# Kernel optimization log

Hardware: AMD Instinct MI355X
Metric: run time of the kernel (lower is better)

Reference implementation:

```python
import jax, jax.numpy as jnp
import numpy as np

S, B, H = 2048, 2, 2048
NH = 16
HD = H // NH  # 128
ROPE_BASE = 10000.0


def _rope_cos_sin(seq_len, dim, dtype):
    inv_freq = 1.0 / (ROPE_BASE ** (jnp.arange(0, dim, 2, dtype=jnp.float32) / dim))
    t = jnp.arange(seq_len, dtype=jnp.float32)
    freqs = jnp.outer(t, inv_freq)            # [S, dim/2]
    emb = jnp.concatenate([freqs, freqs], -1)  # [S, dim]
    return jnp.cos(emb).astype(dtype), jnp.sin(emb).astype(dtype)


def _rotate_half(x):
    x1, x2 = jnp.split(x, 2, axis=-1)
    return jnp.concatenate([-x2, x1], axis=-1)


def setup_inputs() -> dict:
    key = jax.random.key(0)
    k1, k2, k3 = jax.random.split(key, 3)
    hidden_states = jax.random.normal(k1, (S, B, H), dtype=jnp.float32)
    w_qkv = jax.random.normal(k2, (3 * H, H), dtype=jnp.float32) * (1.0 / np.sqrt(H))
    w_out = jax.random.normal(k3, (H, H), dtype=jnp.float32) * (1.0 / np.sqrt(H))
    return {"hidden_states": hidden_states, "w_qkv": w_qkv, "w_out": w_out}


def reference(hidden_states, w_qkv, w_out):
    seq_len, batch, _ = hidden_states.shape
    # QKV projection (nn.Linear: x @ W^T), bias=False
    qkv = jnp.einsum('sbh,oh->sbo', hidden_states, w_qkv)
    qkv = qkv.reshape(seq_len, batch, 3, NH, HD)
    q, k, v = qkv[:, :, 0], qkv[:, :, 1], qkv[:, :, 2]  # [S, B, NH, HD]

    cos, sin = _rope_cos_sin(seq_len, HD, hidden_states.dtype)
    cos = cos[:, None, None, :]
    sin = sin[:, None, None, :]
    q = q * cos + _rotate_half(q) * sin
    k = k * cos + _rotate_half(k) * sin

    # [S, B, NH, HD] -> [B, NH, S, HD]
    q = q.transpose(1, 2, 0, 3)
    k = k.transpose(1, 2, 0, 3)
    v = v.transpose(1, 2, 0, 3)

    scale = 1.0 / np.sqrt(HD)
    scores = jnp.einsum('bhqd,bhkd->bhqk', q, k) * scale
    causal = jnp.tril(jnp.ones((seq_len, seq_len), dtype=bool))
    scores = jnp.where(causal, scores, jnp.finfo(scores.dtype).min)
    probs = jax.nn.softmax(scores, axis=-1)
    attn = jnp.einsum('bhqk,bhkd->bhqd', probs, v)  # [B, NH, S, HD]

    # [B, NH, S, HD] -> [S, B, NH*HD]
    out = attn.transpose(2, 0, 1, 3).reshape(seq_len, batch, -1)
    out = jnp.einsum('sbh,oh->sbo', out, w_out)
    return out
```

## Files before the change

kernel.cpp:

```cpp
#include <hip/hip_runtime.h>
#include <hip/hip_bf16.h>

typedef __attribute__((ext_vector_type(8))) short bf16x8;
typedef __attribute__((ext_vector_type(8))) short s16x8;
typedef __attribute__((ext_vector_type(4))) float f32x4;
typedef __attribute__((ext_vector_type(4))) int i32x4;

#define SEQ 2048
#define BATCH 2
#define HID 2048
#define NH 16
#define HD 128
#define QKVN 6144

static __device__ __forceinline__ short f2bf(float f) {
    union { float f; unsigned u; } v; v.f = f;
    unsigned r = (v.u + 0x7FFFu + ((v.u >> 16) & 1u)) >> 16;
    return (short)r;
}

static __device__ __forceinline__ void gload_lds16(const short* g, short* l) {
    __builtin_amdgcn_global_load_lds((const __attribute__((address_space(1))) void*)g,
                                     (__attribute__((address_space(3))) void*)l, 16, 0, 0);
}

static __device__ __forceinline__ void cvt_body(const float* in, short* out, int i) {
    f32x4 a = *(const f32x4*)(in + (size_t)i * 8);
    f32x4 b = *(const f32x4*)(in + (size_t)i * 8 + 4);
    s16x8 o = { f2bf(a.x), f2bf(a.y), f2bf(a.z), f2bf(a.w),
                f2bf(b.x), f2bf(b.y), f2bf(b.z), f2bf(b.w) };
    *(s16x8*)(out + (size_t)i * 8) = o;
}

__global__ void cvt_kernel(const float* __restrict__ in, short* __restrict__ out, int n8) {
    const int i = blockIdx.x * 256 + threadIdx.x;
    if (i >= n8) return;
    cvt_body(in, out, i);
}

__global__ void cvt2_kernel(const float* __restrict__ inA, short* __restrict__ outA,
                            const float* __restrict__ inB, short* __restrict__ outB) {
    const int bid = blockIdx.x;
    if (bid < 4096) cvt_body(inA, outA, bid * 256 + threadIdx.x);
    else            cvt_body(inB, outB, (bid - 4096) * 256 + threadIdx.x);
}

#define G128_STAGE_A(BUF, HA, KK) do { \
    const short* _s = ((HA) ? aS1 : aS0) + (size_t)(KK) * 64; \
    short* _d = lds + (BUF) * 16384 + (HA) * 8192 + w * 512; \
    gload_lds16(_s, _d); \
    gload_lds16(_s + (size_t)128 * K, _d + 4096); \
} while (0)

#define G128_STAGE_B(BUF, HB, KK) do { \
    const short* _s = ((HB) ? bS1 : bS0) + (size_t)(KK) * 64; \
    short* _d = lds + 32768 + (BUF) * 8192 + (HB) * 4096 + w * 512; \
    gload_lds16(_s, _d); \
} while (0)

#define G128_LOAD_A(HA) do { \
    const short* _p = lds + bufR * 16384 + (HA) * 8192; \
    _Pragma("unroll") \
    for (int mm = 0; mm < 2; ++mm) { \
        aR[mm][0] = *(const bf16x8*)(_p + aOff0 + mm * 1024); \
        aR[mm][1] = *(const bf16x8*)(_p + aOff1 + mm * 1024); \
    } \
} while (0)

#define G128_LOAD_B(HB) do { \
    const short* _p = lds + 32768 + bufR * 8192 + (HB) * 4096; \
    _Pragma("unroll") \
    for (int nn = 0; nn < 2; ++nn) { \
        bR[(HB) * 2 + nn][0] = *(const bf16x8*)(_p + bOff0 + nn * 1024); \
        bR[(HB) * 2 + nn][1] = *(const bf16x8*)(_p + bOff1 + nn * 1024); \
    } \
} while (0)

#define G128_MFMA(HA, HB) do { \
    _Pragma("unroll") \
    for (int mm = 0; mm < 2; ++mm) { \
        _Pragma("unroll") \
        for (int nn = 0; nn < 2; ++nn) { \
            f32x4 _c = acc[(HA) * 2 + mm][(HB) * 2 + nn]; \
            _c = __builtin_amdgcn_mfma_f32_16x16x32_bf16(aR[mm][0], bR[(HB) * 2 + nn][0], _c, 0, 0, 0); \
            _c = __builtin_amdgcn_mfma_f32_16x16x32_bf16(aR[mm][1], bR[(HB) * 2 + nn][1], _c, 0, 0, 0); \
            acc[(HA) * 2 + mm][(HB) * 2 + nn] = _c; \
        } \
    } \
} while (0)

template<bool STORE_BF16>
__global__ __launch_bounds__(512, 2)
void gemm128n(const short* __restrict__ A, const short* __restrict__ B,
              void* __restrict__ Cp, int N, int K) {
    __shared__ short lds[49152];

    const int tid = threadIdx.x;
    const int mBase = blockIdx.y * 256;
    const int nBase = blockIdx.x * 128;
    const int w = tid >> 6, lane = tid & 63, quad = lane >> 4, l15 = lane & 15;
    const int wm = w >> 1, wn = w & 1;

    const int kcol = 8 * ((tid & 7) ^ ((tid >> 3) & 7));
    const int srow = ((tid >> 3) & 15) + (tid >> 7) * 32;
    const short* aS0 = A + (size_t)(mBase + srow) * K + kcol;
    const short* aS1 = aS0 + (size_t)16 * K;
    const short* bS0 = B + (size_t)(nBase + srow) * K + kcol;
    const short* bS1 = bS0 + (size_t)16 * K;

    const int cs0 = (quad * 8) ^ ((l15 & 7) << 3);
    const int aOff0 = (l15 + wm * 32) * 64 + cs0;
    const int aOff1 = aOff0 ^ 32;
    const int bOff0 = (l15 + wn * 32) * 64 + cs0;
    const int bOff1 = bOff0 ^ 32;

    const int NK = K >> 6;
    f32x4 acc[4][4] = {};
    bf16x8 aR[2][2], bR[4][2];

    G128_STAGE_A(0, 0, 0); G128_STAGE_B(0, 0, 0); G128_STAGE_B(0, 1, 0); G128_STAGE_A(0, 1, 0);
    G128_STAGE_A(1, 0, 1); G128_STAGE_B(1, 0, 1); G128_STAGE_B(1, 1, 1);
    asm volatile("s_waitcnt vmcnt(4)" ::: "memory");
    __builtin_amdgcn_s_barrier();

    int bufR = 0;
    for (int k = 0; k < NK; ++k) {
        const int kk1 = (k + 1 < NK) ? k + 1 : NK - 1;
        const int kk2 = (k + 2 < NK) ? k + 2 : NK - 1;
        G128_LOAD_A(0);
        G128_LOAD_B(0);
        G128_STAGE_A(bufR ^ 1, 1, kk1);
        asm volatile("s_waitcnt lgkmcnt(4)" ::: "memory");
        __builtin_amdgcn_s_barrier();
        asm volatile("s_waitcnt lgkmcnt(0)" ::: "memory");
        __builtin_amdgcn_s_setprio(1);
        G128_MFMA(0, 0);
        __builtin_amdgcn_s_setprio(0);
        __builtin_amdgcn_s_barrier();
        G128_LOAD_B(1);
        G128_STAGE_A(bufR, 0, kk2);
        __builtin_amdgcn_s_barrier();
        asm volatile("s_waitcnt lgkmcnt(0)" ::: "memory");
        __builtin_amdgcn_s_setprio(1);
        G128_MFMA(0, 1);
        __builtin_amdgcn_s_setprio(0);
        __builtin_amdgcn_s_barrier();
        G128_LOAD_A(1);
        G128_STAGE_B(bufR, 0, kk2);
        __builtin_amdgcn_s_barrier();
        asm volatile("s_waitcnt lgkmcnt(0)" ::: "memory");
        __builtin_amdgcn_s_setprio(1);
        G128_MFMA(1, 1);
        __builtin_amdgcn_s_setprio(0);
        __builtin_amdgcn_s_barrier();
        G128_STAGE_B(bufR, 1, kk2);
        asm volatile("s_waitcnt vmcnt(4)" ::: "memory");
        __builtin_amdgcn_s_barrier();
        __builtin_amdgcn_s_setprio(1);
        G128_MFMA(1, 0);
        __builtin_amdgcn_s_setprio(0);
        __builtin_amdgcn_s_barrier();
        bufR ^= 1;
    }
    asm volatile("s_waitcnt vmcnt(0)" ::: "memory");

    #pragma unroll
    for (int af = 0; af < 4; ++af) {
        const int ha = af >> 1, mm = af & 1;
        const int row0 = mBase + wm * 64 + (2 * mm + ha) * 16 + quad * 4;
        #pragma unroll
        for (int bg = 0; bg < 4; ++bg) {
            const int hb = bg >> 1, nn = bg & 1;
            const int col = nBase + wn * 64 + (2 * nn + hb) * 16 + l15;
            #pragma unroll
            for (int r = 0; r < 4; ++r) {
                if (STORE_BF16)
                    ((short*)Cp)[(size_t)(row0 + r) * N + col] = f2bf(acc[af][bg][r]);
                else
                    ((float*)Cp)[(size_t)(row0 + r) * N + col] = acc[af][bg][r];
            }
        }
    }
}

__global__ void rope_kernel(short* __restrict__ qkv) {
    const int tid = blockIdx.x * 256 + threadIdx.x;
    const int d     = tid & 63;
    const int h     = (tid >> 6) & 15;
    const int which = (tid >> 10) & 1;
    const int b     = (tid >> 11) & 1;
    const int s     = tid >> 12;

    const size_t base = (size_t)(s * 2 + b) * QKVN + which * 2048 + h * 128;
    const float inv_freq = expf(-((float)(2 * d) * (1.0f / 128.0f)) * 9.210340371976184f);
    float sn, cs;
    sincosf((float)s * inv_freq, &sn, &cs);
    const float post = (which == 0) ? 0.08838834764831845f : 1.0f;

    union { unsigned u; float f; } x1, x2;
    x1.u = ((unsigned)(unsigned short)qkv[base + d]) << 16;
    x2.u = ((unsigned)(unsigned short)qkv[base + d + 64]) << 16;
    qkv[base + d]      = f2bf((x1.f * cs - x2.f * sn) * post);
    qkv[base + d + 64] = f2bf((x2.f * cs + x1.f * sn) * post);
}

__global__ void vtrans_kernel(const short* __restrict__ qkv, short* __restrict__ vT) {
    __shared__ short T[64][72];
    const int s0 = blockIdx.x * 64, d0 = blockIdx.y * 64;
    const int bh = blockIdx.z;
    const int b = bh >> 4, h = bh & 15;
    const int t = threadIdx.x;

    #pragma unroll
    for (int p = 0; p < 2; ++p) {
        const int sl = (t >> 3) + p * 32;
        const int dl = (t & 7) * 8;
        *(i32x4*)&T[sl][dl] =
            *(const i32x4*)(qkv + (size_t)((s0 + sl) * 2 + b) * QKVN + 4096 + h * 128 + d0 + dl);
    }
    __syncthreads();
    #pragma unroll
    for (int p = 0; p < 2; ++p) {
        const int dl = (t >> 3) + p * 32;
        const int sl = (t & 7) * 8;
        short tmp[8];
        #pragma unroll
        for (int j = 0; j < 8; ++j) tmp[j] = T[sl + j][dl];
        *(i32x4*)(vT + ((size_t)bh * 128 + d0 + dl) * 2048 + s0 + sl) = *(i32x4*)tmp;
    }
}

__global__ __launch_bounds__(256, 2)
void attn_kernel(const short* __restrict__ qkv, const short* __restrict__ vT,
                 short* __restrict__ out) {
    __shared__ short lds[40960];

    const int bx = blockIdx.x;
    const int h = blockIdx.y, b = blockIdx.z;
    const int Aq = (bx & 1) ? (bx >> 1) : (15 - (bx >> 1));
    const int qt = b ? (15 - Aq) : Aq;
    const int tid = threadIdx.x;
    const int w = tid >> 6, lane = tid & 63, quad = lane >> 4, l15 = lane & 15;
    const int bh = b * 16 + h;
    const int cswz = (l15 & 7) << 3;

    bf16x8 aq[2][4];
    #pragma unroll
    for (int m = 0; m < 2; ++m) {
        const short* qbase =
            qkv + (size_t)((qt * 128 + w * 32 + m * 16 + l15) * 2 + b) * QKVN + h * 128;
        #pragma unroll
        for (int c = 0; c < 4; ++c)
            aq[m][c] = *(const bf16x8*)(qbase + c * 32 + quad * 8);
    }

    f32x4 oacc[2][8] = {};
    float lpart[2][4] = {};

    const short* kSrc0 = qkv + (size_t)((w * 16 + (lane >> 4)) * 2 + b) * QKVN
                       + 2048 + h * 128 + ((lane & 15) ^ (lane >> 4)) * 8;
    const short* kSrc1 = qkv + (size_t)((w * 16 + 4 + (lane >> 4)) * 2 + b) * QKVN
                       + 2048 + h * 128 + ((lane & 15) ^ (4 | (lane >> 4))) * 8;
    const short* vSrc = vT + ((size_t)bh * 128 + w * 32 + (lane >> 3)) * 2048
                      + ((lane & 7) ^ ((lane >> 3) & 7)) * 8;
    short* kDst = lds + w * 2048;
    short* vDst = lds + 16384 + w * 2048;

#define STAGE_KV(BUF, KK0) do { \
    const size_t kAdv = (size_t)(KK0) * 2 * QKVN; \
    short* _kd = kDst + (BUF) * 8192; \
    short* _vd = vDst + (BUF) * 8192; \
    gload_lds16(kSrc0 + kAdv,                  _kd); \
    gload_lds16(kSrc1 + kAdv,                  _kd + 512); \
    gload_lds16(kSrc0 + kAdv + 16 * QKVN,      _kd + 1024); \
    gload_lds16(kSrc1 + kAdv + 16 * QKVN,      _kd + 1536); \
    gload_lds16(vSrc + (KK0),                  _vd); \
    gload_lds16(vSrc + (KK0) + 8 * 2048,       _vd + 512); \
    gload_lds16(vSrc + (KK0) + 16 * 2048,      _vd + 1024); \
    gload_lds16(vSrc + (KK0) + 24 * 2048,      _vd + 1536); \
} while (0)

    const int nChunks = 2 * qt + 2;

    STAGE_KV(0, 0);
    asm volatile("s_waitcnt vmcnt(0)" ::: "memory");
    __builtin_amdgcn_s_barrier();

    for (int ck = 0; ck < nChunks; ++ck) {
        const int cur = ck & 1;
        const int kk0 = ck * 64;
        if (ck + 1 < nChunks) STAGE_KV(cur ^ 1, kk0 + 64);

        const short* Kc = lds + cur * 8192;
        const short* Vc = lds + 16384 + cur * 8192;
        short* Pw = lds + 32768 + w * 2048;

        f32x4 sc4[2][4] = {};
        #pragma unroll
        for (int c = 0; c < 4; ++c) {
            const int cb = (c * 32 + quad * 8) ^ cswz;
            #pragma unroll
            for (int n = 0; n < 4; ++n) {
                bf16x8 bk = *(const bf16x8*)(Kc + (n * 16 + l15) * 128 + cb);
                sc4[0][n] = __builtin_amdgcn_mfma_f32_16x16x32_bf16(aq[0][c], bk, sc4[0][n], 0, 0, 0);
                sc4[1][n] = __builtin_amdgcn_mfma_f32_16x16x32_bf16(aq[1][c], bk, sc4[1][n], 0, 0, 0);
            }
        }

        const bool diag = (ck >= 2 * qt);
        #pragma unroll
        for (int m = 0; m < 2; ++m) {
            const int rowbase = qt * 128 + w * 32 + m * 16 + quad * 4;
            #pragma unroll
            for (int r = 0; r < 4; ++r) {
                const int prow = m * 16 + quad * 4 + r;
                const int pswz = ((quad * 4 + r) & 7) << 3;
                #pragma unroll
                for (int n = 0; n < 4; ++n) {
                    float sv = sc4[m][n][r];
                    if (diag && (kk0 + n * 16 + l15 > rowbase + r)) sv = -1e30f;
                    const float p = __expf(sv);
                    lpart[m][r] += p;
                    Pw[prow * 64 + ((n * 16 + l15) ^ pswz)] = f2bf(p);
                }
            }
        }

        #pragma unroll
        for (int kp2 = 0; kp2 < 2; ++kp2) {
            const int cb = (kp2 * 32 + quad * 8) ^ cswz;
            bf16x8 ap0 = *(const bf16x8*)(Pw + l15 * 64 + cb);
            bf16x8 ap1 = *(const bf16x8*)(Pw + (16 + l15) * 64 + cb);
            #pragma unroll
            for (int dt = 0; dt < 8; ++dt) {
                bf16x8 bv = *(const bf16x8*)(Vc + (dt * 16 + l15) * 64 + cb);
                oacc[0][dt] = __builtin_amdgcn_mfma_f32_16x16x32_bf16(ap0, bv, oacc[0][dt], 0, 0, 0);
                oacc[1][dt] = __builtin_amdgcn_mfma_f32_16x16x32_bf16(ap1, bv, oacc[1][dt], 0, 0, 0);
            }
        }

        asm volatile("s_waitcnt vmcnt(0)" ::: "memory");
        __builtin_amdgcn_s_barrier();
    }
#undef STAGE_KV

    #pragma unroll
    for (int m = 0; m < 2; ++m) {
        const int rowbase = qt * 128 + w * 32 + m * 16 + quad * 4;
        #pragma unroll
        for (int r = 0; r < 4; ++r) {
            float l = lpart[m][r];
            #pragma unroll
            for (int off = 1; off < 16; off <<= 1)
                l += __shfl_xor(l, off);
            const float inv_l = 1.0f / l;
            const size_t obase = (size_t)((rowbase + r) * 2 + b) * HID + h * 128;
            #pragma unroll
            for (int dt = 0; dt < 8; ++dt)
                out[obase + dt * 16 + l15] = f2bf(oacc[m][dt][r] * inv_l);
        }
    }
}

extern "C" void kernel_launch(void* const* d_in, const int* in_sizes, int n_in,
                              void* d_out, int out_size, void* d_ws, size_t ws_size,
                              hipStream_t stream) {
    const float* hidden = (const float*)d_in[0];
    const float* w_qkv  = (const float*)d_in[1];
    const float* w_out  = (const float*)d_in[2];
    float* out = (float*)d_out;

    short* qkv     = (short*)d_ws;
    short* attnb   = qkv + (size_t)4096 * QKVN;
    short* wqkv_bf = attnb + (size_t)4096 * HID;
    short* wout_bf = wqkv_bf;
    short* hbf     = wqkv_bf + (size_t)QKVN * HID;
    short* vT      = hbf;

    dim3 blk(256);
    cvt2_kernel<<<dim3(4096 + 6144), blk, 0, stream>>>(hidden, hbf, w_qkv, wqkv_bf);
    gemm128n<true><<<dim3(QKVN / 128, 4096 / 256), dim3(512), 0, stream>>>(
        hbf, wqkv_bf, qkv, QKVN, HID);
    cvt_kernel<<<dim3(2048), blk, 0, stream>>>(w_out, wout_bf, 2048 * 256);
    rope_kernel<<<dim3((SEQ * BATCH * 2 * NH * (HD / 2)) / 256), blk, 0, stream>>>(qkv);
    vtrans_kernel<<<dim3(SEQ / 64, HD / 64, BATCH * NH), blk, 0, stream>>>(qkv, vT);
    attn_kernel<<<dim3(SEQ / 128, NH, BATCH), blk, 0, stream>>>(qkv, vT, attnb);
    gemm128n<false><<<dim3(HID / 128, 4096 / 256), dim3(512), 0, stream>>>(
        attnb, wout_bf, out, HID, HID);
}
```

Baseline: 362.3 us.

## Fuse RoPE and Q scaling into QKV GEMM epilogue via remapped B columns

Changes the B-fragment mapping so that each wave holds columns d and d+64 of the same 128-wide head tile, which lets the QKV GEMM epilogue apply the rotary embedding and the Q softmax scale directly from registers. The separate rope kernel, along with its read-modify-write pass over Q and K, is removed. The epilogue now computes expf and sincosf per element group and stores with a different column pattern, which adds transcendental work and may reduce store coalescing.

After: 346.4 us. -4.4%, faster.

```diff
diff --git a/kernel.cpp b/kernel.cpp
--- a/kernel.cpp
+++ b/kernel.cpp
@@ -71,8 +71,8 @@
     const short* _p = lds + 32768 + bufR * 8192 + (HB) * 4096; \
     _Pragma("unroll") \
     for (int nn = 0; nn < 2; ++nn) { \
-        bR[(HB) * 2 + nn][0] = *(const bf16x8*)(_p + bOff0 + nn * 1024); \
-        bR[(HB) * 2 + nn][1] = *(const bf16x8*)(_p + bOff1 + nn * 1024); \
+        bR[(HB) * 2 + nn][0] = *(const bf16x8*)(_p + bOff0 + nn * 2048); \
+        bR[(HB) * 2 + nn][1] = *(const bf16x8*)(_p + bOff1 + nn * 2048); \
     } \
 } while (0)
 
@@ -89,7 +89,7 @@
     } \
 } while (0)
 
-template<bool STORE_BF16>
+template<int MODE>
 __global__ __launch_bounds__(512, 2)
 void gemm128n(const short* __restrict__ A, const short* __restrict__ B,
               void* __restrict__ Cp, int N, int K) {
@@ -111,7 +111,7 @@
     const int cs0 = (quad * 8) ^ ((l15 & 7) << 3);
     const int aOff0 = (l15 + wm * 32) * 64 + cs0;
     const int aOff1 = aOff0 ^ 32;
-    const int bOff0 = (l15 + wn * 32) * 64 + cs0;
+    const int bOff0 = (l15 + wn * 16) * 64 + cs0;
     const int bOff1 = bOff0 ^ 32;
 
     const int NK = K >> 6;
@@ -164,44 +164,54 @@
     }
     asm volatile("s_waitcnt vmcnt(0)" ::: "memory");
 
-    #pragma unroll
-    for (int af = 0; af < 4; ++af) {
-        const int ha = af >> 1, mm = af & 1;
-        const int row0 = mBase + wm * 64 + (2 * mm + ha) * 16 + quad * 4;
-        #pragma unroll
-        for (int bg = 0; bg < 4; ++bg) {
-            const int hb = bg >> 1, nn = bg & 1;
-            const int col = nBase + wn * 64 + (2 * nn + hb) * 16 + l15;
-            #pragma unroll
-            for (int r = 0; r < 4; ++r) {
-                if (STORE_BF16)
-                    ((short*)Cp)[(size_t)(row0 + r) * N + col] = f2bf(acc[af][bg][r]);
-                else
-                    ((float*)Cp)[(size_t)(row0 + r) * N + col] = acc[af][bg][r];
-            }
-        }
-    }
-}
-
-__global__ void rope_kernel(short* __restrict__ qkv) {
-    const int tid = blockIdx.x * 256 + threadIdx.x;
-    const int d     = tid & 63;
-    const int h     = (tid >> 6) & 15;
-    const int which = (tid >> 10) & 1;
-    const int b     = (tid >> 11) & 1;
-    const int s     = tid >> 12;
-
-    const size_t base = (size_t)(s * 2 + b) * QKVN + which * 2048 + h * 128;
-    const float inv_freq = expf(-((float)(2 * d) * (1.0f / 128.0f)) * 9.210340371976184f);
-    float sn, cs;
-    sincosf((float)s * inv_freq, &sn, &cs);
-    const float post = (which == 0) ? 0.08838834764831845f : 1.0f;
-
-    union { unsigned u; float f; } x1, x2;
-    x1.u = ((unsigned)(unsigned short)qkv[base + d]) << 16;
-    x2.u = ((unsigned)(unsigned short)qkv[base + d + 64]) << 16;
-    qkv[base + d]      = f2bf((x1.f * cs - x2.f * sn) * post);
-    qkv[base + d + 64] = f2bf((x2.f * cs + x1.f * sn) * post);
+    if (MODE == 1 && nBase < 4096) {
+        const float post = (nBase < 2048) ? 0.08838834764831845f : 1.0f;
+        short* C = (short*)Cp;
+        #pragma unroll
+        for (int af = 0; af < 4; ++af) {
+            const int ha = af >> 1, mm = af & 1;
+            const int row0 = mBase + wm * 64 + (2 * mm + ha) * 16 + quad * 4;
+            #pragma unroll
+            for (int hb = 0; hb < 2; ++hb) {
+                const int d = wn * 32 + hb * 16 + l15;
+                const float inv_freq =
+                    expf(-((float)(2 * d) * (1.0f / 128.0f)) * 9.210340371976184f);
+                #pragma unroll
+                for (int rp = 0; rp < 2; ++rp) {
+                    const int s = (row0 >> 1) + rp;
+                    float sn, cs;
+                    sincosf((float)s * inv_freq, &sn, &cs);
+                    #pragma unroll
+                    for (int rr = 0; rr < 2; ++rr) {
+                        const int r = rp * 2 + rr;
+                        const float x1 = acc[af][hb * 2 + 0][r];
+                        const float x2 = acc[af][hb * 2 + 1][r];
+                        const size_t rb = (size_t)(row0 + r) * N + nBase + d;
+                        C[rb]      = f2bf((x1 * cs - x2 * sn) * post);
+                        C[rb + 64] = f2bf((x2 * cs + x1 * sn) * post);
+                    }
+                }
+            }
+        }
+    } else {
+        #pragma unroll
+        for (int af = 0; af < 4; ++af) {
+            const int ha = af >> 1, mm = af & 1;
+            const int row0 = mBase + wm * 64 + (2 * mm + ha) * 16 + quad * 4;
+            #pragma unroll
+            for (int bg = 0; bg < 4; ++bg) {
+                const int hb = bg >> 1, nn = bg & 1;
+                const int col = nBase + nn * 64 + wn * 32 + hb * 16 + l15;
+                #pragma unroll
+                for (int r = 0; r < 4; ++r) {
+                    if (MODE == 1)
+                        ((short*)Cp)[(size_t)(row0 + r) * N + col] = f2bf(acc[af][bg][r]);
+                    else
+                        ((float*)Cp)[(size_t)(row0 + r) * N + col] = acc[af][bg][r];
+                }
+            }
+        }
+    }
 }
 
 __global__ void vtrans_kernel(const short* __restrict__ qkv, short* __restrict__ vT) {
@@ -379,12 +389,11 @@
 
     dim3 blk(256);
     cvt2_kernel<<<dim3(4096 + 6144), blk, 0, stream>>>(hidden, hbf, w_qkv, wqkv_bf);
-    gemm128n<true><<<dim3(QKVN / 128, 4096 / 256), dim3(512), 0, stream>>>(
+    gemm128n<1><<<dim3(QKVN / 128, 4096 / 256), dim3(512), 0, stream>>>(
         hbf, wqkv_bf, qkv, QKVN, HID);
     cvt_kernel<<<dim3(2048), blk, 0, stream>>>(w_out, wout_bf, 2048 * 256);
-    rope_kernel<<<dim3((SEQ * BATCH * 2 * NH * (HD / 2)) / 256), blk, 0, stream>>>(qkv);
     vtrans_kernel<<<dim3(SEQ / 64, HD / 64, BATCH * NH), blk, 0, stream>>>(qkv, vT);
     attn_kernel<<<dim3(SEQ / 128, NH, BATCH), blk, 0, stream>>>(qkv, vT, attnb);
-    gemm128n<false><<<dim3(HID / 128, 4096 / 256), dim3(512), 0, stream>>>(
+    gemm128n<0><<<dim3(HID / 128, 4096 / 256), dim3(512), 0, stream>>>(
         attnb, wout_bf, out, HID, HID);
 }
```
